# Kernel tuning notes

Hardware: AMD Instinct MI355X
Metric: run time of the kernel (lower is better)

## Reference

```python
import jax, jax.numpy as jnp
import numpy as np

EPS = 1e-12


def _gather_neighbors(t, idx):
    # t: (bs, v, d), idx: (bs, v, n) -> (bs, v, n, d)  [torch: t[arange(bs)[:,None,None], idx]]
    bs, v, n = idx.shape
    flat = jnp.take_along_axis(t, idx.reshape(bs, v * n)[..., None], axis=1)
    return flat.reshape(bs, v, n, t.shape[-1])


def setup_inputs() -> dict:
    key = jax.random.key(0)
    ks = jax.random.split(key, 9)
    bs, v, n, inc, outc, sup = 8, 2048, 20, 64, 128, 2
    return {
        "neighbor_index": jax.random.randint(ks[0], (bs, v, n), 0, v),
        "vertices": jax.random.normal(ks[1], (bs, v, 3), dtype=jnp.float32),
        "feature_map": jax.random.normal(ks[2], (bs, v, inc), dtype=jnp.float32),
        "weights": jax.random.normal(ks[3], (inc, (sup + 1) * outc), dtype=jnp.float32) * 0.05,
        "bias": jax.random.normal(ks[4], ((sup + 1) * outc,), dtype=jnp.float32) * 0.05,
        "directions": jax.random.normal(ks[5], (3, sup * outc), dtype=jnp.float32) * 0.05,
        "distance_w": jax.random.normal(ks[6], (1, sup * outc), dtype=jnp.float32) * 0.05,
        "mlp_w": jax.random.normal(ks[7], (outc, 2 * outc), dtype=jnp.float32) * 0.05,
        "mlp_b": jax.random.normal(ks[8], (outc,), dtype=jnp.float32) * 0.05,
    }


def reference(neighbor_index, vertices, feature_map, weights, bias, directions, distance_w, mlp_w, mlp_b):
    bs, v, n = neighbor_index.shape
    outc = mlp_w.shape[0]
    sup = directions.shape[1] // outc

    # neighbor directions and distances (single gather, reuse norm)
    neighbors = _gather_neighbors(vertices, neighbor_index)          # (bs,v,n,3)
    direction = neighbors - vertices[:, :, None, :]                  # (bs,v,n,3)
    dist = jnp.linalg.norm(direction, axis=-1)                       # (bs,v,n)
    dir_norm = direction / jnp.maximum(dist[..., None], EPS)         # F.normalize
    dist_max = jnp.max(dist, axis=2, keepdims=True)                  # (bs,v,1)

    # support directions normalized along dim 0
    sdn = directions / jnp.maximum(jnp.linalg.norm(directions, axis=0, keepdims=True), EPS)
    theta = jax.nn.relu(jnp.einsum('bvnc,cs->bvns', dir_norm, sdn))  # (bs,v,n,sup*outc)
    dist_feat = jax.nn.relu(dist_max @ distance_w)                   # (bs,v,sup*outc)

    feat = feature_map @ weights + bias                              # (bs,v,(sup+1)*outc)
    center = feat[..., :outc]
    support = feat[..., outc:]
    support_g = _gather_neighbors(support, neighbor_index)           # (bs,v,n,sup*outc)

    act = (theta * support_g).reshape(bs, v, n, sup, outc)
    act = jnp.sum(jnp.max(act, axis=2), axis=2)                      # max over neighbors, sum over supports
    fuse = center + act                                              # (bs,v,outc)
    dist_sum = jnp.sum(dist_feat.reshape(bs, v, sup, outc), axis=2)  # (bs,v,outc)

    out = jnp.concatenate([fuse, dist_sum], axis=-1)                 # (bs,v,2*outc)
    return out @ mlp_w.T + mlp_b                                     # (bs,v,outc)
```

## Files before the change

kernel.cpp:

```cpp
#include <hip/hip_runtime.h>
#include <hip/hip_bf16.h>

#define BS    8
#define V     2048
#define NNB   20
#define INC   64
#define OUTC  128
#define SUP   2
#define NCOL  ((SUP + 1) * OUTC)
#define SCOL  (SUP * OUTC)
#define ROWS  (BS * V)

using bf16x8 = __bf16 __attribute__((ext_vector_type(8)));
using bf16x4 = __bf16 __attribute__((ext_vector_type(4)));
using f32x4  = float  __attribute__((ext_vector_type(4)));
using f32x2  = float  __attribute__((ext_vector_type(2)));
using i32x4  = int    __attribute__((ext_vector_type(4)));
using u16x4  = unsigned short __attribute__((ext_vector_type(4)));

#if __has_builtin(__builtin_elementwise_fma)
static __device__ inline f32x2 efma(f32x2 a, f32x2 b, f32x2 c) { return __builtin_elementwise_fma(a, b, c); }
#else
static __device__ inline f32x2 efma(f32x2 a, f32x2 b, f32x2 c) {
    f32x2 r; r[0] = fmaf(a[0], b[0], c[0]); r[1] = fmaf(a[1], b[1], c[1]); return r;
}
#endif
#if __has_builtin(__builtin_elementwise_max)
static __device__ inline f32x2 emax(f32x2 a, f32x2 b) { return __builtin_elementwise_max(a, b); }
#else
static __device__ inline f32x2 emax(f32x2 a, f32x2 b) {
    f32x2 r; r[0] = fmaxf(a[0], b[0]); r[1] = fmaxf(a[1], b[1]); return r;
}
#endif

static __device__ inline bf16x8 cvt8(f32x4 lo, f32x4 hi) {
    bf16x8 r;
    r[0] = (__bf16)lo[0]; r[1] = (__bf16)lo[1]; r[2] = (__bf16)lo[2]; r[3] = (__bf16)lo[3];
    r[4] = (__bf16)hi[0]; r[5] = (__bf16)hi[1]; r[6] = (__bf16)hi[2]; r[7] = (__bf16)hi[3];
    return r;
}

static __device__ inline float b2f(unsigned short u) {
    union { unsigned int i; float f; } c; c.i = ((unsigned int)u) << 16; return c.f;
}

__global__ __launch_bounds__(256) void k_prep(const float* __restrict__ W,
                                              const float* __restrict__ Wm,
                                              const float* __restrict__ dw,
                                              __bf16* __restrict__ WTb,
                                              __bf16* __restrict__ Wm1b,
                                              float* __restrict__ w2) {
    const int b = blockIdx.x;
    if (b < 96) {
        const int idx = b * 256 + threadIdx.x;
        const int c = idx >> 6, k = idx & 63;
        WTb[idx] = (__bf16)W[k * NCOL + c];
    } else if (b < 160) {
        const int idx = (b - 96) * 256 + threadIdx.x;
        const int o = idx >> 7, k = idx & 127;
        Wm1b[idx] = (__bf16)Wm[o * SCOL + k];
    } else {
        __shared__ float u[OUTC];
        const int t = threadIdx.x;
        if (t < OUTC) u[t] = fmaxf(dw[t], 0.f) + fmaxf(dw[OUTC + t], 0.f);
        __syncthreads();
        if (t < OUTC) {
            float s = 0.f;
            for (int k = 0; k < OUTC; ++k) s = fmaf(Wm[t * SCOL + OUTC + k], u[k], s);
            w2[t] = s;
        }
    }
}

__global__ __launch_bounds__(256) void k_feat(const float* __restrict__ fm,
                                              const __bf16* __restrict__ WTb,
                                              const float* __restrict__ bias,
                                              float* __restrict__ center,
                                              __bf16* __restrict__ supb) {
    const int row0 = blockIdx.x * 32;
    const int wid = threadIdx.x >> 6, lane = threadIdx.x & 63;
    const int ln = lane & 15, lg = lane >> 4;
    const int cbase = wid * 96;

    bf16x8 a[2][2];
#pragma unroll
    for (int rs = 0; rs < 2; ++rs) {
        const float* ap = fm + (size_t)(row0 + rs * 16 + ln) * INC + lg * 8;
        a[rs][0] = cvt8(*(const f32x4*)(ap +  0), *(const f32x4*)(ap +  4));
        a[rs][1] = cvt8(*(const f32x4*)(ap + 32), *(const f32x4*)(ap + 36));
    }

    f32x4 acc[2][6];
#pragma unroll
    for (int t = 0; t < 6; ++t) {
        const float bb = bias[cbase + t * 16 + ln];
        acc[0][t] = (f32x4){bb, bb, bb, bb};
        acc[1][t] = acc[0][t];
    }

    const __bf16* bp = WTb + (size_t)(cbase + ln) * INC + lg * 8;
#pragma unroll
    for (int t = 0; t < 6; ++t) {
        const bf16x8 b0 = *(const bf16x8*)(bp + t * 16 * INC);
        const bf16x8 b1 = *(const bf16x8*)(bp + t * 16 * INC + 32);
        acc[0][t] = __builtin_amdgcn_mfma_f32_16x16x32_bf16(a[0][0], b0, acc[0][t], 0, 0, 0);
        acc[0][t] = __builtin_amdgcn_mfma_f32_16x16x32_bf16(a[0][1], b1, acc[0][t], 0, 0, 0);
        acc[1][t] = __builtin_amdgcn_mfma_f32_16x16x32_bf16(a[1][0], b0, acc[1][t], 0, 0, 0);
        acc[1][t] = __builtin_amdgcn_mfma_f32_16x16x32_bf16(a[1][1], b1, acc[1][t], 0, 0, 0);
    }

#pragma unroll
    for (int rs = 0; rs < 2; ++rs) {
        const int r0 = row0 + rs * 16 + lg * 4;
#pragma unroll
        for (int t = 0; t < 6; ++t) {
            const int col = cbase + t * 16 + ln;
            if (col < OUTC) {
#pragma unroll
                for (int r = 0; r < 4; ++r)
                    center[(size_t)(r0 + r) * OUTC + col] = acc[rs][t][r];
            } else {
                const int sc = col - OUTC;
#pragma unroll
                for (int r = 0; r < 4; ++r)
                    supb[(size_t)(r0 + r) * SCOL + sc] = (__bf16)acc[rs][t][r];
            }
        }
    }
}

__global__ __launch_bounds__(256, 4) void k_neigh(const int*   __restrict__ nbr,
                                                  const float* __restrict__ verts,
                                                  const float* __restrict__ dirs,
                                                  const float* __restrict__ center,
                                                  const __bf16* __restrict__ supb,
                                                  __bf16* __restrict__ Xb,
                                                  float* __restrict__ dmaxv) {
    const int bid   = blockIdx.x;
    const int batch = bid & 7;
    const int chunk = bid >> 3;
    const int wid   = threadIdx.x >> 6;
    const int lane  = threadIdx.x & 63;
    const int half  = lane >> 5;
    const int sl    = lane & 31;
    const int u     = chunk * 8 + wid * 2 + half;
    const int bV    = batch * V;
    const int row   = bV + u;
    const int c0    = sl * 4;

    __shared__ float vlds[V][4];

    for (int i = threadIdx.x; i < V * 3; i += 256) {
        const int vv = i / 3, cc = i - vv * 3;
        vlds[vv][cc] = verts[(size_t)bV * 3 + i];
    }

    f32x4 A0 = *(const f32x4*)(dirs +            c0);
    f32x4 A1 = *(const f32x4*)(dirs + SCOL +     c0);
    f32x4 A2 = *(const f32x4*)(dirs + 2*SCOL +   c0);
    f32x4 B0 = *(const f32x4*)(dirs +            OUTC + c0);
    f32x4 B1 = *(const f32x4*)(dirs + SCOL +     OUTC + c0);
    f32x4 B2 = *(const f32x4*)(dirs + 2*SCOL +   OUTC + c0);
#pragma unroll
    for (int j = 0; j < 4; ++j) {
        float inv = __builtin_amdgcn_rsqf(fmaxf(fmaf(A0[j], A0[j], fmaf(A1[j], A1[j], A2[j]*A2[j])), 1e-24f));
        A0[j] *= inv; A1[j] *= inv; A2[j] *= inv;
        inv = __builtin_amdgcn_rsqf(fmaxf(fmaf(B0[j], B0[j], fmaf(B1[j], B1[j], B2[j]*B2[j])), 1e-24f));
        B0[j] *= inv; B1[j] *= inv; B2[j] *= inv;
    }
    const f32x2 ax0 = {A0[0], A0[1]}, ax1 = {A0[2], A0[3]};
    const f32x2 ay0 = {A1[0], A1[1]}, ay1 = {A1[2], A1[3]};
    const f32x2 az0 = {A2[0], A2[1]}, az1 = {A2[2], A2[3]};
    const f32x2 bx0 = {B0[0], B0[1]}, bx1 = {B0[2], B0[3]};
    const f32x2 by0 = {B1[0], B1[1]}, by1 = {B1[2], B1[3]};
    const f32x2 bz0 = {B2[0], B2[1]}, bz1 = {B2[2], B2[3]};
    const f32x2 zero = {0.f, 0.f};

    int gs[NNB];
    {
        const i32x4* np4 = reinterpret_cast<const i32x4*>(nbr + (size_t)row * NNB);
#pragma unroll
        for (int t = 0; t < 5; ++t) {
            const i32x4 g4 = np4[t];
            gs[t*4+0] = g4[0]; gs[t*4+1] = g4[1]; gs[t*4+2] = g4[2]; gs[t*4+3] = g4[3];
        }
    }

    __syncthreads();

    const float vx = vlds[u][0], vy = vlds[u][1], vz = vlds[u][2];

    f32x2 mA0 = {-INFINITY, -INFINITY}, mA1 = mA0, mB0 = mA0, mB1 = mA0;
    float d2max = 0.f;
    const __bf16* supBase = supb + (size_t)bV * SCOL + c0;

#pragma unroll
    for (int t = 0; t < 4; ++t) {
        u16x4 s0r[5], s1r[5];
        f32x4 vl[5];
#pragma unroll
        for (int q = 0; q < 5; ++q) {
            const int g = gs[t * 5 + q];
            const __bf16* sg = supBase + (size_t)g * SCOL;
            s0r[q] = *(const u16x4*)(sg);
            s1r[q] = *(const u16x4*)(sg + OUTC);
            vl[q]  = *(const f32x4*)&vlds[g][0];
        }
#pragma unroll
        for (int q = 0; q < 5; ++q) {
            const float dx = vl[q][0] - vx, dy = vl[q][1] - vy, dz = vl[q][2] - vz;
            const float d2 = fmaf(dx, dx, fmaf(dy, dy, dz * dz));
            d2max = fmaxf(d2max, d2);
            const float inv = __builtin_amdgcn_rsqf(fmaxf(d2, 1e-24f));
            const f32x2 nX = {dx * inv, dx * inv};
            const f32x2 nY = {dy * inv, dy * inv};
            const f32x2 nZ = {dz * inv, dz * inv};

            const f32x2 s0lo = {b2f(s0r[q][0]), b2f(s0r[q][1])};
            const f32x2 s0hi = {b2f(s0r[q][2]), b2f(s0r[q][3])};
            const f32x2 s1lo = {b2f(s1r[q][0]), b2f(s1r[q][1])};
            const f32x2 s1hi = {b2f(s1r[q][2]), b2f(s1r[q][3])};

            const f32x2 tA0 = emax(efma(nZ, az0, efma(nY, ay0, nX * ax0)), zero);
            const f32x2 tA1 = emax(efma(nZ, az1, efma(nY, ay1, nX * ax1)), zero);
            const f32x2 tB0 = emax(efma(nZ, bz0, efma(nY, by0, nX * bx0)), zero);
            const f32x2 tB1 = emax(efma(nZ, bz1, efma(nY, by1, nX * bx1)), zero);
            mA0 = emax(mA0, tA0 * s0lo);
            mA1 = emax(mA1, tA1 * s0hi);
            mB0 = emax(mB0, tB0 * s1lo);
            mB1 = emax(mB1, tB1 * s1hi);
        }
    }

    const f32x4 cc = *(const f32x4*)(center + (size_t)row * OUTC + c0);
    const f32x2 f01 = (f32x2){cc[0], cc[1]} + mA0 + mB0;
    const f32x2 f23 = (f32x2){cc[2], cc[3]} + mA1 + mB1;
    bf16x4 fx;
    fx[0] = (__bf16)f01[0]; fx[1] = (__bf16)f01[1];
    fx[2] = (__bf16)f23[0]; fx[3] = (__bf16)f23[1];
    *(bf16x4*)(Xb + (size_t)row * OUTC + c0) = fx;
    if (sl == 0) dmaxv[row] = sqrtf(d2max);
}

__global__ __launch_bounds__(256) void k_out(const __bf16* __restrict__ Xb,
                                             const __bf16* __restrict__ Wm1b,
                                             const float* __restrict__ dmaxv,
                                             const float* __restrict__ w2,
                                             const float* __restrict__ mb,
                                             float* __restrict__ out) {
    const int wid = threadIdx.x >> 6, lane = threadIdx.x & 63;
    const int ln = lane & 15, lg = lane >> 4;
    const int row0 = blockIdx.x * 32 + (wid >> 1) * 16;
    const int cb = (wid & 1) * 64;

    const __bf16* ap = Xb + (size_t)(row0 + ln) * OUTC + lg * 8;
    bf16x8 a[4];
#pragma unroll
    for (int kf = 0; kf < 4; ++kf) a[kf] = *(const bf16x8*)(ap + kf * 32);

    f32x4 acc[4];
#pragma unroll
    for (int t = 0; t < 4; ++t) acc[t] = (f32x4)0.f;

    const __bf16* bp = Wm1b + (size_t)(cb + ln) * OUTC + lg * 8;
#pragma unroll
    for (int t = 0; t < 4; ++t) {
#pragma unroll
        for (int kf = 0; kf < 4; ++kf) {
            const bf16x8 b = *(const bf16x8*)(bp + t * 16 * OUTC + kf * 32);
            acc[t] = __builtin_amdgcn_mfma_f32_16x16x32_bf16(a[kf], b, acc[t], 0, 0, 0);
        }
    }

    float dm[4];
#pragma unroll
    for (int r = 0; r < 4; ++r) dm[r] = dmaxv[row0 + lg * 4 + r];

#pragma unroll
    for (int t = 0; t < 4; ++t) {
        const int col = cb + t * 16 + ln;
        const float w2c = w2[col];
        const float bb = mb[col];
#pragma unroll
        for (int r = 0; r < 4; ++r)
            out[(size_t)(row0 + lg * 4 + r) * OUTC + col] = fmaf(dm[r], w2c, acc[t][r] + bb);
    }
}

extern "C" void kernel_launch(void* const* d_in, const int* in_sizes, int n_in,
                              void* d_out, int out_size, void* d_ws, size_t ws_size,
                              hipStream_t stream) {
    const int*   nbr   = (const int*)  d_in[0];
    const float* verts = (const float*)d_in[1];
    const float* fm    = (const float*)d_in[2];
    const float* W     = (const float*)d_in[3];
    const float* bias  = (const float*)d_in[4];
    const float* dirs  = (const float*)d_in[5];
    const float* dw    = (const float*)d_in[6];
    const float* Wm    = (const float*)d_in[7];
    const float* mb    = (const float*)d_in[8];
    float* out = (float*)d_out;

    float*  center  = (float*)d_ws;
    __bf16* supb    = (__bf16*)(center + (size_t)ROWS * OUTC);
    __bf16* Xb      = supb + (size_t)ROWS * SCOL;
    float*  dmaxv   = (float*)(Xb + (size_t)ROWS * OUTC);
    __bf16* WTb     = (__bf16*)(dmaxv + ROWS);
    __bf16* Wm1b    = WTb + NCOL * INC;
    float*  w2      = (float*)(Wm1b + OUTC * OUTC);

    k_prep <<<161,        256, 0, stream>>>(W, Wm, dw, WTb, Wm1b, w2);
    k_feat <<<ROWS / 32,  256, 0, stream>>>(fm, WTb, bias, center, supb);
    k_neigh<<<ROWS / 8,   256, 0, stream>>>(nbr, verts, dirs, center, supb, Xb, dmaxv);
    k_out  <<<ROWS / 32,  256, 0, stream>>>(Xb, Wm1b, dmaxv, w2, mb, out);
}
```

Measured before the change: 124.4 us.

## Fuse neighbor aggregation with output MLP and drop per-block vertex LDS staging

Merges the neighbor max-aggregation kernel and the output MFMA projection into one kernel. Each block now handles 16 rows, stages the bf16 fused features and max distances in LDS, and runs the 128x128 projection directly from there. This removes the global round trip for the intermediate X/dmax buffers and one launch. It also stops copying each batch's full 2048-vertex table into LDS per block and reads neighbor vertices straight from global memory instead. That trades LDS staging for uncached scattered 12-byte global reads.

```diff
diff --git a/kernel.cpp b/kernel.cpp
--- a/kernel.cpp
+++ b/kernel.cpp
@@ -10,6 +10,7 @@
 #define NCOL  ((SUP + 1) * OUTC)
 #define SCOL  (SUP * OUTC)
 #define ROWS  (BS * V)
+#define XPAD  136
 
 using bf16x8 = __bf16 __attribute__((ext_vector_type(8)));
 using bf16x4 = __bf16 __attribute__((ext_vector_type(4)));
@@ -129,31 +130,30 @@
     }
 }
 
-__global__ __launch_bounds__(256, 4) void k_neigh(const int*   __restrict__ nbr,
-                                                  const float* __restrict__ verts,
-                                                  const float* __restrict__ dirs,
-                                                  const float* __restrict__ center,
-                                                  const __bf16* __restrict__ supb,
-                                                  __bf16* __restrict__ Xb,
-                                                  float* __restrict__ dmaxv) {
+__global__ __launch_bounds__(256, 4) void k_no(const int*   __restrict__ nbr,
+                                               const float* __restrict__ verts,
+                                               const float* __restrict__ dirs,
+                                               const float* __restrict__ center,
+                                               const __bf16* __restrict__ supb,
+                                               const __bf16* __restrict__ Wm1b,
+                                               const float* __restrict__ w2,
+                                               const float* __restrict__ mb,
+                                               float* __restrict__ out) {
     const int bid   = blockIdx.x;
     const int batch = bid & 7;
     const int chunk = bid >> 3;
-    const int wid   = threadIdx.x >> 6;
-    const int lane  = threadIdx.x & 63;
+    const int u0    = chunk * 16;
+    const int bV    = batch * V;
+    const int tid   = threadIdx.x;
+    const int wid   = tid >> 6;
+    const int lane  = tid & 63;
     const int half  = lane >> 5;
     const int sl    = lane & 31;
-    const int u     = chunk * 8 + wid * 2 + half;
-    const int bV    = batch * V;
-    const int row   = bV + u;
     const int c0    = sl * 4;
-
-    __shared__ float vlds[V][4];
-
-    for (int i = threadIdx.x; i < V * 3; i += 256) {
-        const int vv = i / 3, cc = i - vv * 3;
-        vlds[vv][cc] = verts[(size_t)bV * 3 + i];
-    }
+    const int ln    = lane & 15, lg = lane >> 4;
+
+    __shared__ __bf16 Xl[16][XPAD];
+    __shared__ float  dl[16];
 
     f32x4 A0 = *(const f32x4*)(dirs +            c0);
     f32x4 A1 = *(const f32x4*)(dirs + SCOL +     c0);
@@ -176,114 +176,115 @@
     const f32x2 bz0 = {B2[0], B2[1]}, bz1 = {B2[2], B2[3]};
     const f32x2 zero = {0.f, 0.f};
 
-    int gs[NNB];
+    const __bf16* supBase = supb + (size_t)bV * SCOL + c0;
+
+#pragma unroll
+    for (int p = 0; p < 2; ++p) {
+        const int ul  = p * 8 + wid * 2 + half;
+        const int row = bV + u0 + ul;
+
+        const float vx = verts[row * 3 + 0];
+        const float vy = verts[row * 3 + 1];
+        const float vz = verts[row * 3 + 2];
+
+        int gs[NNB];
+        {
+            const i32x4* np4 = reinterpret_cast<const i32x4*>(nbr + (size_t)row * NNB);
+#pragma unroll
+            for (int t = 0; t < 5; ++t) {
+                const i32x4 g4 = np4[t];
+                gs[t*4+0] = g4[0]; gs[t*4+1] = g4[1]; gs[t*4+2] = g4[2]; gs[t*4+3] = g4[3];
+            }
+        }
+
+        f32x2 mA0 = {-INFINITY, -INFINITY}, mA1 = mA0, mB0 = mA0, mB1 = mA0;
+        float d2max = 0.f;
+
+#pragma unroll
+        for (int t = 0; t < 4; ++t) {
+            u16x4 s0r[5], s1r[5];
+            float px[5], py[5], pz[5];
+#pragma unroll
+            for (int q = 0; q < 5; ++q) {
+                const int g = gs[t * 5 + q];
+                const __bf16* sg = supBase + (size_t)g * SCOL;
+                s0r[q] = *(const u16x4*)(sg);
+                s1r[q] = *(const u16x4*)(sg + OUTC);
+                const float* vp = verts + (size_t)(bV + g) * 3;
+                px[q] = vp[0]; py[q] = vp[1]; pz[q] = vp[2];
+            }
+#pragma unroll
+            for (int q = 0; q < 5; ++q) {
+                const float dx = px[q] - vx, dy = py[q] - vy, dz = pz[q] - vz;
+                const float d2 = fmaf(dx, dx, fmaf(dy, dy, dz * dz));
+                d2max = fmaxf(d2max, d2);
+                const float inv = __builtin_amdgcn_rsqf(fmaxf(d2, 1e-24f));
+                const f32x2 nX = {dx * inv, dx * inv};
+                const f32x2 nY = {dy * inv, dy * inv};
+                const f32x2 nZ = {dz * inv, dz * inv};
+
+                const f32x2 s0lo = {b2f(s0r[q][0]), b2f(s0r[q][1])};
+                const f32x2 s0hi = {b2f(s0r[q][2]), b2f(s0r[q][3])};
+                const f32x2 s1lo = {b2f(s1r[q][0]), b2f(s1r[q][1])};
+                const f32x2 s1hi = {b2f(s1r[q][2]), b2f(s1r[q][3])};
+
+                const f32x2 tA0 = emax(efma(nZ, az0, efma(nY, ay0, nX * ax0)), zero);
+                const f32x2 tA1 = emax(efma(nZ, az1, efma(nY, ay1, nX * ax1)), zero);
+                const f32x2 tB0 = emax(efma(nZ, bz0, efma(nY, by0, nX * bx0)), zero);
+                const f32x2 tB1 = emax(efma(nZ, bz1, efma(nY, by1, nX * bx1)), zero);
+                mA0 = emax(mA0, tA0 * s0lo);
+                mA1 = emax(mA1, tA1 * s0hi);
+                mB0 = emax(mB0, tB0 * s1lo);
+                mB1 = emax(mB1, tB1 * s1hi);
+            }
+        }
+
+        const f32x4 cc = *(const f32x4*)(center + (size_t)row * OUTC + c0);
+        const f32x2 f01 = (f32x2){cc[0], cc[1]} + mA0 + mB0;
+        const f32x2 f23 = (f32x2){cc[2], cc[3]} + mA1 + mB1;
+        bf16x4 fx;
+        fx[0] = (__bf16)f01[0]; fx[1] = (__bf16)f01[1];
+        fx[2] = (__bf16)f23[0]; fx[3] = (__bf16)f23[1];
+        *(bf16x4*)(&Xl[ul][c0]) = fx;
+        if (sl == 0) dl[ul] = sqrtf(d2max);
+    }
+    __syncthreads();
+
     {
-        const i32x4* np4 = reinterpret_cast<const i32x4*>(nbr + (size_t)row * NNB);
-#pragma unroll
-        for (int t = 0; t < 5; ++t) {
-            const i32x4 g4 = np4[t];
-            gs[t*4+0] = g4[0]; gs[t*4+1] = g4[1]; gs[t*4+2] = g4[2]; gs[t*4+3] = g4[3];
-        }
-    }
-
-    __syncthreads();
-
-    const float vx = vlds[u][0], vy = vlds[u][1], vz = vlds[u][2];
-
-    f32x2 mA0 = {-INFINITY, -INFINITY}, mA1 = mA0, mB0 = mA0, mB1 = mA0;
-    float d2max = 0.f;
-    const __bf16* supBase = supb + (size_t)bV * SCOL + c0;
-
-#pragma unroll
-    for (int t = 0; t < 4; ++t) {
-        u16x4 s0r[5], s1r[5];
-        f32x4 vl[5];
-#pragma unroll
-        for (int q = 0; q < 5; ++q) {
-            const int g = gs[t * 5 + q];
-            const __bf16* sg = supBase + (size_t)g * SCOL;
-            s0r[q] = *(const u16x4*)(sg);
-            s1r[q] = *(const u16x4*)(sg + OUTC);
-            vl[q]  = *(const f32x4*)&vlds[g][0];
-        }
-#pragma unroll
-        for (int q = 0; q < 5; ++q) {
-            const float dx = vl[q][0] - vx, dy = vl[q][1] - vy, dz = vl[q][2] - vz;
-            const float d2 = fmaf(dx, dx, fmaf(dy, dy, dz * dz));
-            d2max = fmaxf(d2max, d2);
-            const float inv = __builtin_amdgcn_rsqf(fmaxf(d2, 1e-24f));
-            const f32x2 nX = {dx * inv, dx * inv};
-            const f32x2 nY = {dy * inv, dy * inv};
-            const f32x2 nZ = {dz * inv, dz * inv};
-
-            const f32x2 s0lo = {b2f(s0r[q][0]), b2f(s0r[q][1])};
-            const f32x2 s0hi = {b2f(s0r[q][2]), b2f(s0r[q][3])};
-            const f32x2 s1lo = {b2f(s1r[q][0]), b2f(s1r[q][1])};
-            const f32x2 s1hi = {b2f(s1r[q][2]), b2f(s1r[q][3])};
-
-            const f32x2 tA0 = emax(efma(nZ, az0, efma(nY, ay0, nX * ax0)), zero);
-            const f32x2 tA1 = emax(efma(nZ, az1, efma(nY, ay1, nX * ax1)), zero);
-            const f32x2 tB0 = emax(efma(nZ, bz0, efma(nY, by0, nX * bx0)), zero);
-            const f32x2 tB1 = emax(efma(nZ, bz1, efma(nY, by1, nX * bx1)), zero);
-            mA0 = emax(mA0, tA0 * s0lo);
-            mA1 = emax(mA1, tA1 * s0hi);
-            mB0 = emax(mB0, tB0 * s1lo);
-            mB1 = emax(mB1, tB1 * s1hi);
-        }
-    }
-
-    const f32x4 cc = *(const f32x4*)(center + (size_t)row * OUTC + c0);
-    const f32x2 f01 = (f32x2){cc[0], cc[1]} + mA0 + mB0;
-    const f32x2 f23 = (f32x2){cc[2], cc[3]} + mA1 + mB1;
-    bf16x4 fx;
-    fx[0] = (__bf16)f01[0]; fx[1] = (__bf16)f01[1];
-    fx[2] = (__bf16)f23[0]; fx[3] = (__bf16)f23[1];
-    *(bf16x4*)(Xb + (size_t)row * OUTC + c0) = fx;
-    if (sl == 0) dmaxv[row] = sqrtf(d2max);
-}
-
-__global__ __launch_bounds__(256) void k_out(const __bf16* __restrict__ Xb,
-                                             const __bf16* __restrict__ Wm1b,
-                                             const float* __restrict__ dmaxv,
-                                             const float* __restrict__ w2,
-                                             const float* __restrict__ mb,
-                                             float* __restrict__ out) {
-    const int wid = threadIdx.x >> 6, lane = threadIdx.x & 63;
-    const int ln = lane & 15, lg = lane >> 4;
-    const int row0 = blockIdx.x * 32 + (wid >> 1) * 16;
-    const int cb = (wid & 1) * 64;
-
-    const __bf16* ap = Xb + (size_t)(row0 + ln) * OUTC + lg * 8;
-    bf16x8 a[4];
-#pragma unroll
-    for (int kf = 0; kf < 4; ++kf) a[kf] = *(const bf16x8*)(ap + kf * 32);
-
-    f32x4 acc[4];
-#pragma unroll
-    for (int t = 0; t < 4; ++t) acc[t] = (f32x4)0.f;
-
-    const __bf16* bp = Wm1b + (size_t)(cb + ln) * OUTC + lg * 8;
-#pragma unroll
-    for (int t = 0; t < 4; ++t) {
-#pragma unroll
-        for (int kf = 0; kf < 4; ++kf) {
-            const bf16x8 b = *(const bf16x8*)(bp + t * 16 * OUTC + kf * 32);
-            acc[t] = __builtin_amdgcn_mfma_f32_16x16x32_bf16(a[kf], b, acc[t], 0, 0, 0);
-        }
-    }
-
-    float dm[4];
-#pragma unroll
-    for (int r = 0; r < 4; ++r) dm[r] = dmaxv[row0 + lg * 4 + r];
-
-#pragma unroll
-    for (int t = 0; t < 4; ++t) {
-        const int col = cb + t * 16 + ln;
-        const float w2c = w2[col];
-        const float bb = mb[col];
-#pragma unroll
-        for (int r = 0; r < 4; ++r)
-            out[(size_t)(row0 + lg * 4 + r) * OUTC + col] = fmaf(dm[r], w2c, acc[t][r] + bb);
+        const int cb = wid * 32;
+
+        bf16x8 a[4];
+#pragma unroll
+        for (int kf = 0; kf < 4; ++kf)
+            a[kf] = *(const bf16x8*)(&Xl[ln][lg * 8 + kf * 32]);
+
+        f32x4 acc[2];
+        acc[0] = (f32x4)0.f; acc[1] = (f32x4)0.f;
+
+        const __bf16* bp = Wm1b + (size_t)(cb + ln) * OUTC + lg * 8;
+#pragma unroll
+        for (int t = 0; t < 2; ++t) {
+#pragma unroll
+            for (int kf = 0; kf < 4; ++kf) {
+                const bf16x8 b = *(const bf16x8*)(bp + t * 16 * OUTC + kf * 32);
+                acc[t] = __builtin_amdgcn_mfma_f32_16x16x32_bf16(a[kf], b, acc[t], 0, 0, 0);
+            }
+        }
+
+        float dm[4];
+#pragma unroll
+        for (int r = 0; r < 4; ++r) dm[r] = dl[lg * 4 + r];
+
+        const int rowg0 = bV + u0 + lg * 4;
+#pragma unroll
+        for (int t = 0; t < 2; ++t) {
+            const int col = cb + t * 16 + ln;
+            const float w2c = w2[col];
+            const float bb  = mb[col];
+#pragma unroll
+            for (int r = 0; r < 4; ++r)
+                out[(size_t)(rowg0 + r) * OUTC + col] = fmaf(dm[r], w2c, acc[t][r] + bb);
+        }
     }
 }
 
@@ -303,14 +304,11 @@
 
     float*  center  = (float*)d_ws;
     __bf16* supb    = (__bf16*)(center + (size_t)ROWS * OUTC);
-    __bf16* Xb      = supb + (size_t)ROWS * SCOL;
-    float*  dmaxv   = (float*)(Xb + (size_t)ROWS * OUTC);
-    __bf16* WTb     = (__bf16*)(dmaxv + ROWS);
+    __bf16* WTb     = supb + (size_t)ROWS * SCOL;
     __bf16* Wm1b    = WTb + NCOL * INC;
     float*  w2      = (float*)(Wm1b + OUTC * OUTC);
 
     k_prep <<<161,        256, 0, stream>>>(W, Wm, dw, WTb, Wm1b, w2);
     k_feat <<<ROWS / 32,  256, 0, stream>>>(fm, WTb, bias, center, supb);
-    k_neigh<<<ROWS / 8,   256, 0, stream>>>(nbr, verts, dirs, center, supb, Xb, dmaxv);
-    k_out  <<<ROWS / 32,  256, 0, stream>>>(Xb, Wm1b, dmaxv, w2, mb, out);
-}
+    k_no   <<<ROWS / 16,  256, 0, stream>>>(nbr, verts, dirs, center, supb, Wm1b, w2, mb, out);
+}
```

Result: faster. 117.3 us (-5.7%).
